# Kernel tuning notes

Hardware: AMD Instinct MI355X
Metric: run time of the kernel (lower is better)

The kernel has to match this reference:

```python
import jax, jax.numpy as jnp
import numpy as np

B, S, E, H = 4, 2048, 1024, 16
D = E // H  # head dim = 64


def setup_inputs() -> dict:
    key = jax.random.key(0)
    ks = jax.random.split(key, 8)
    scale = 0.02
    return {
        "query": jax.random.normal(ks[0], (B, S, E), jnp.float32),
        "keys": jax.random.normal(ks[1], (B, S, E), jnp.float32),
        "values": jax.random.normal(ks[2], (B, S, E), jnp.float32),
        "mask": jnp.ones((B, 1, 1, S), jnp.int32),
        "Wq": jax.random.normal(ks[3], (D, D), jnp.float32) * scale,
        "Wk": jax.random.normal(ks[4], (D, D), jnp.float32) * scale,
        "Wv": jax.random.normal(ks[5], (D, D), jnp.float32) * scale,
        "Wf": jax.random.normal(ks[6], (E, E), jnp.float32) * scale,
        "bf": jax.random.normal(ks[7], (E,), jnp.float32) * scale,
    }


def reference(query, keys, values, mask, Wq, Wk, Wv, Wf, bf):
    b, sq, _ = query.shape
    sk = keys.shape[1]
    # reshape to heads: [b, s, H, D]
    q = query.reshape(b, sq, H, D)
    k = keys.reshape(b, sk, H, D)
    v = values.reshape(b, sk, H, D)
    # per-head linear projections (torch Linear: x @ W.T, no bias)
    q = jnp.einsum('bshd,ed->bshe', q, Wq)
    k = jnp.einsum('bshd,ed->bshe', k, Wk)
    v = jnp.einsum('bshd,ed->bshe', v, Wv)
    # scores [b, h, q, k]
    scores = jnp.einsum('bqhd,bkhd->bhqk', q, k)
    scores = jnp.where(mask == 0, -jnp.inf, scores)
    attn = jax.nn.softmax(scores / jnp.sqrt(jnp.float32(D)), axis=3)
    # context [b, q, h, d] -> [b, q, E]
    ctx = jnp.einsum('bhqk,bkhd->bqhd', attn, v).reshape(b, sq, E)
    return ctx @ Wf.T + bf
```

## Files before the change

kernel.cpp:

```cpp
#include <hip/hip_runtime.h>

#define B_ 4
#define S_ 2048
#define E_ 1024
#define H_ 16
#define D_ 64

typedef unsigned short u16;
typedef unsigned int u32;
typedef __bf16 bf16x8 __attribute__((ext_vector_type(8)));
typedef __bf16 bf16x4 __attribute__((ext_vector_type(4)));
typedef float f32x4 __attribute__((ext_vector_type(4)));
typedef u16 u16x8 __attribute__((ext_vector_type(8)));
typedef u16 u16x4 __attribute__((ext_vector_type(4)));

#if defined(__has_builtin)
#if __has_builtin(__builtin_amdgcn_exp2f)
#define EXP2F(x) __builtin_amdgcn_exp2f(x)
#else
#define EXP2F(x) exp2f(x)
#endif
#else
#define EXP2F(x) exp2f(x)
#endif

__device__ __forceinline__ u16 bfbits(float f) {
  __bf16 h = (__bf16)f;
  return __builtin_bit_cast(u16, h);
}
__device__ __forceinline__ f32x4 mfma16(bf16x8 a, bf16x8 b, f32x4 c) {
  return __builtin_amdgcn_mfma_f32_16x16x32_bf16(a, b, c, 0, 0, 0);
}
__device__ __forceinline__ bf16x8 lds_ld8(const u16* base, int off) {
  return *reinterpret_cast<const bf16x8*>(reinterpret_cast<const char*>(base) + off);
}
__device__ __forceinline__ bf16x4 lds_ld4(const u16* base, int off) {
  return *reinterpret_cast<const bf16x4*>(reinterpret_cast<const char*>(base) + off);
}
__device__ __forceinline__ void gload_lds16(const u16* g, u16* l) {
  __builtin_amdgcn_global_load_lds((const __attribute__((address_space(1))) void*)g,
                                   (__attribute__((address_space(3))) void*)l, 16, 0, 0);
}

__global__ __launch_bounds__(256) void proj_kernel(
    const float* __restrict__ qin, const float* __restrict__ kin, const float* __restrict__ vin,
    const float* __restrict__ Wq, const float* __restrict__ Wk, const float* __restrict__ Wv,
    u16* __restrict__ qo, u16* __restrict__ ko, u16* __restrict__ vo)
{
  __shared__ __align__(16) u16 Al[128 * 64];
  __shared__ __align__(16) u16 Wl[64 * 64];
  const int t = threadIdx.x, w = t >> 6, l = t & 63, lg = l >> 4, ln = l & 15;
  const int tensor = blockIdx.z >> 2, b = blockIdx.z & 3;
  const int h = blockIdx.y, s0 = blockIdx.x * 128;

  const float* x; const float* W; float scale;
  if (tensor == 0)      { x = qin; W = Wq; scale = 0.125f * 1.44269504f; }
  else if (tensor == 1) { x = kin; W = Wk; scale = 1.0f; }
  else                  { x = vin; W = Wv; scale = 1.0f; }

  {
    const int e = t >> 2, d0 = (t & 3) * 16;
    const float4* wr = reinterpret_cast<const float4*>(W + e * 64 + d0);
    float4 f0 = wr[0], f1 = wr[1], f2 = wr[2], f3 = wr[3];
    u16x8 p0, p1;
    p0[0]=bfbits(f0.x*scale); p0[1]=bfbits(f0.y*scale); p0[2]=bfbits(f0.z*scale); p0[3]=bfbits(f0.w*scale);
    p0[4]=bfbits(f1.x*scale); p0[5]=bfbits(f1.y*scale); p0[6]=bfbits(f1.z*scale); p0[7]=bfbits(f1.w*scale);
    p1[0]=bfbits(f2.x*scale); p1[1]=bfbits(f2.y*scale); p1[2]=bfbits(f2.z*scale); p1[3]=bfbits(f2.w*scale);
    p1[4]=bfbits(f3.x*scale); p1[5]=bfbits(f3.y*scale); p1[6]=bfbits(f3.z*scale); p1[7]=bfbits(f3.w*scale);
    *reinterpret_cast<u16x8*>(reinterpret_cast<char*>(Wl) + ((e*128 + d0*2     ) ^ ((e & 7) << 4))) = p0;
    *reinterpret_cast<u16x8*>(reinterpret_cast<char*>(Wl) + ((e*128 + d0*2 + 16) ^ ((e & 7) << 4))) = p1;
  }
  {
    const int row = t >> 1, d0 = (t & 1) * 32;
    const float4* xr = reinterpret_cast<const float4*>(x + ((size_t)(b * S_ + s0 + row)) * E_ + h * D_ + d0);
    #pragma unroll
    for (int c = 0; c < 4; ++c) {
      float4 f0 = xr[2 * c], f1 = xr[2 * c + 1];
      u16x8 pk;
      pk[0]=bfbits(f0.x); pk[1]=bfbits(f0.y); pk[2]=bfbits(f0.z); pk[3]=bfbits(f0.w);
      pk[4]=bfbits(f1.x); pk[5]=bfbits(f1.y); pk[6]=bfbits(f1.z); pk[7]=bfbits(f1.w);
      *reinterpret_cast<u16x8*>(reinterpret_cast<char*>(Al) +
          ((row * 128 + (d0 + 8 * c) * 2) ^ ((row & 7) << 4))) = pk;
    }
  }
  __syncthreads();

  bf16x8 wb[4][2];
  #pragma unroll
  for (int nn = 0; nn < 4; ++nn) {
    int brow = nn * 16 + ln;
    int bo = (brow * 128 + lg * 16) ^ ((ln & 7) << 4);
    wb[nn][0] = lds_ld8(Wl, bo);
    wb[nn][1] = lds_ld8(Wl, bo ^ 64);
  }
  f32x4 acc[2][4] = {};
  #pragma unroll
  for (int sub = 0; sub < 2; ++sub) {
    int arow = 32 * w + 16 * sub + ln;
    int ao = (arow * 128 + lg * 16) ^ ((ln & 7) << 4);
    bf16x8 a0 = lds_ld8(Al, ao), a1 = lds_ld8(Al, ao ^ 64);
    #pragma unroll
    for (int nn = 0; nn < 4; ++nn) {
      acc[sub][nn] = mfma16(a0, wb[nn][0], acc[sub][nn]);
      acc[sub][nn] = mfma16(a1, wb[nn][1], acc[sub][nn]);
    }
  }

  if (tensor < 2) {
    u16* o = (tensor == 0) ? qo : ko;
    const size_t hb = ((size_t)(b * H_ + h)) * (S_ * D_);
    #pragma unroll
    for (int sub = 0; sub < 2; ++sub)
      #pragma unroll
      for (int nn = 0; nn < 4; ++nn)
        #pragma unroll
        for (int r = 0; r < 4; ++r)
          o[hb + (size_t)(s0 + 32*w + 16*sub + 4*lg + r) * D_ + nn*16 + ln] = bfbits(acc[sub][nn][r]);
  } else {
    const size_t hb = ((size_t)(b * H_ + h)) * (D_ * S_);
    #pragma unroll
    for (int sub = 0; sub < 2; ++sub)
      #pragma unroll
      for (int nn = 0; nn < 4; ++nn)
        #pragma unroll
        for (int r = 0; r < 4; ++r)
          vo[hb + (size_t)(nn*16 + ln) * S_ + s0 + 32*w + 16*sub + 4*lg + r] = bfbits(acc[sub][nn][r]);
  }
}

__global__ __launch_bounds__(256) void cvt_kernel(const float* __restrict__ in, u16* __restrict__ o)
{
  int i = blockIdx.x * 256 + threadIdx.x;
  float4 f = reinterpret_cast<const float4*>(in)[i];
  u16x4 h4;
  h4[0] = bfbits(f.x); h4[1] = bfbits(f.y); h4[2] = bfbits(f.z); h4[3] = bfbits(f.w);
  reinterpret_cast<u16x4*>(o)[i] = h4;
}

__global__ __launch_bounds__(512, 4) void attn_kernel(
    const u16* __restrict__ qw,
    const u16* __restrict__ kw,
    const u16* __restrict__ vtw,
    const int* __restrict__ mask,
    u16* __restrict__ ctx)
{
  __shared__ __align__(16) u16 Kl[2][64 * 64];
  __shared__ __align__(16) u16 Vl[2][64 * 64];
  __shared__ int s_allone;

  const int t = threadIdx.x, w = t >> 6, l = t & 63, lg = l >> 4, ln = l & 15;
  const int hb = blockIdx.x;
  const int b = hb >> 4;
  const int q0 = blockIdx.y * 256;
  const size_t koff = (size_t)hb * (S_ * D_);
  const size_t voff = (size_t)hb * (D_ * S_);

  if (t == 0) s_allone = 1;
  __syncthreads();

  const int srow = t >> 3, scol = (t & 7) ^ ((t >> 3) & 7);
  const u16* kg = kw + koff + srow * D_ + scol * 8;
  const u16* vg = vtw + voff + (size_t)srow * S_ + scol * 8;
  u16* kd = &Kl[0][0] + t * 8;
  u16* vd = &Vl[0][0] + t * 8;

  gload_lds16(kg, kd);
  gload_lds16(vg, vd);

  {
    const int4 m4 = *reinterpret_cast<const int4*>(mask + b * S_ + t * 4);
    if (!(m4.x && m4.y && m4.z && m4.w)) s_allone = 0;
  }

  bf16x8 qb[2][2];
  #pragma unroll
  for (int sub = 0; sub < 2; ++sub) {
    const u16* qp = qw + koff + (size_t)(q0 + 32*w + 16*sub + ln) * D_ + 8*lg;
    qb[sub][0] = *reinterpret_cast<const bf16x8*>(qp);
    qb[sub][1] = *reinterpret_cast<const bf16x8*>(qp + 32);
  }

  f32x4 oacc[2][4] = {};
  float l_s[2] = {0.f, 0.f};

  asm volatile("s_waitcnt vmcnt(0)" ::: "memory");
  __syncthreads();
  const int allone = s_allone;

  int cur = 0;
  for (int kt = 0; kt < S_ / 64; ++kt) {
    if (kt + 1 < S_ / 64) {
      const int nk = (kt + 1) * 64;
      gload_lds16(kg + nk * D_, kd + (cur ^ 1) * 4096);
      gload_lds16(vg + nk,      vd + (cur ^ 1) * 4096);
    }
    const u16* Kc = &Kl[cur][0];
    const u16* Vc = &Vl[cur][0];

    f32x4 sc[2][4];
    __builtin_amdgcn_s_setprio(1);
    #pragma unroll
    for (int kn = 0; kn < 4; ++kn) {
      int o0 = (ln * 128 + lg * 16) ^ ((ln & 7) << 4);
      o0 += kn * 2048;
      bf16x8 ka0 = lds_ld8(Kc, o0), ka1 = lds_ld8(Kc, o0 ^ 64);
      #pragma unroll
      for (int sub = 0; sub < 2; ++sub) {
        f32x4 z = {0.f, 0.f, 0.f, 0.f};
        z = mfma16(ka0, qb[sub][0], z);
        z = mfma16(ka1, qb[sub][1], z);
        sc[sub][kn] = z;
      }
    }
    __builtin_amdgcn_s_setprio(0);

    if (!allone) {
      const int kv0 = kt * 64;
      #pragma unroll
      for (int kn = 0; kn < 4; ++kn) {
        const int4 m4 = *reinterpret_cast<const int4*>(mask + b * S_ + kv0 + kn * 16 + lg * 4);
        const int* mp = reinterpret_cast<const int*>(&m4);
        #pragma unroll
        for (int r = 0; r < 4; ++r)
          if (mp[r] == 0) { sc[0][kn][r] = -1e30f; sc[1][kn][r] = -1e30f; }
      }
    }

    bf16x8 pa[2][2];
    #pragma unroll
    for (int sub = 0; sub < 2; ++sub) {
      float ps = 0.f;
      #pragma unroll
      for (int kn = 0; kn < 4; ++kn)
        #pragma unroll
        for (int r = 0; r < 4; ++r) {
          float p = EXP2F(sc[sub][kn][r]);
          ps += p;
          pa[sub][kn >> 1][(kn & 1) * 4 + r] = (__bf16)p;
        }
      l_s[sub] += ps;
    }

    __builtin_amdgcn_s_setprio(1);
    #pragma unroll
    for (int kh = 0; kh < 2; ++kh) {
      bf16x8 vb[4];
      #pragma unroll
      for (int dn = 0; dn < 4; ++dn) {
        int vo0 = ((ln * 128 + 8 * lg + 64 * kh) ^ ((ln & 7) << 4)) + dn * 2048;
        bf16x4 v0 = lds_ld4(Vc, vo0);
        bf16x4 v1 = lds_ld4(Vc, vo0 ^ 32);
        vb[dn] = __builtin_shufflevector(v0, v1, 0, 1, 2, 3, 4, 5, 6, 7);
      }
      #pragma unroll
      for (int sub = 0; sub < 2; ++sub)
        #pragma unroll
        for (int dn = 0; dn < 4; ++dn)
          oacc[sub][dn] = mfma16(pa[sub][kh], vb[dn], oacc[sub][dn]);
    }
    __builtin_amdgcn_s_setprio(0);

    if (kt + 1 < S_ / 64) {
      asm volatile("s_waitcnt vmcnt(0)" ::: "memory");
      __syncthreads();
      cur ^= 1;
    }
  }

  #pragma unroll
  for (int sub = 0; sub < 2; ++sub) {
    l_s[sub] += __shfl_xor(l_s[sub], 16, 64);
    l_s[sub] += __shfl_xor(l_s[sub], 32, 64);
    float linv = 1.f / l_s[sub];
    #pragma unroll
    for (int r = 0; r < 4; ++r) {
      float lr = __shfl(linv, 4 * lg + r, 64);
      int qrow = q0 + 32 * w + 16 * sub + 4 * lg + r;
      size_t base = ((size_t)b * S_ + qrow) * E_ + (hb & 15) * D_;
      #pragma unroll
      for (int dn = 0; dn < 4; ++dn)
        ctx[base + dn * 16 + ln] = bfbits(oacc[sub][dn][r] * lr);
    }
  }
}

__global__ __launch_bounds__(256, 2) void outproj_kernel(
    const u16* __restrict__ ctx, const u16* __restrict__ wf,
    const float* __restrict__ bias, float* __restrict__ out)
{
  __shared__ __align__(16) u16 Al[2][128 * 64];
  __shared__ __align__(16) u16 Bl[2][128 * 64];
  const int t = threadIdx.x, w = t >> 6, l = t & 63, lg = l >> 4, ln = l & 15;
  const int wm = w >> 1, wn = w & 1;
  const int m0 = blockIdx.x * 128, n0 = blockIdx.y * 128;
  f32x4 acc[4][4] = {};

  const u16* ag[4]; const u16* bg[4]; int ldo[4];
  #pragma unroll
  for (int it = 0; it < 4; ++it) {
    int j = it * 256 + t, row = j >> 3, c = (j & 7) ^ (row & 7);
    ag[it] = ctx + (size_t)(m0 + row) * E_ + c * 8;
    bg[it] = wf  + (size_t)(n0 + row) * E_ + c * 8;
    ldo[it] = j * 8;
  }
  #pragma unroll
  for (int it = 0; it < 4; ++it) {
    gload_lds16(ag[it], &Al[0][0] + ldo[it]);
    gload_lds16(bg[it], &Bl[0][0] + ldo[it]);
  }
  asm volatile("s_waitcnt vmcnt(0)" ::: "memory");
  __syncthreads();

  int cur = 0;
  for (int kt = 0; kt < E_ / 64; ++kt) {
    if (kt + 1 < E_ / 64) {
      const int k0 = (kt + 1) * 64;
      #pragma unroll
      for (int it = 0; it < 4; ++it) {
        gload_lds16(ag[it] + k0, &Al[cur ^ 1][0] + ldo[it]);
        gload_lds16(bg[it] + k0, &Bl[cur ^ 1][0] + ldo[it]);
      }
    }
    const u16* Ac = &Al[cur][0]; const u16* Bc = &Bl[cur][0];

    bf16x8 af[4][2], bff[4][2];
    #pragma unroll
    for (int ms = 0; ms < 4; ++ms) {
      int ar = 64 * wm + 16 * ms + ln;
      int ao = (ar * 128 + lg * 16) ^ ((ln & 7) << 4);
      af[ms][0] = lds_ld8(Ac, ao); af[ms][1] = lds_ld8(Ac, ao ^ 64);
    }
    #pragma unroll
    for (int ns = 0; ns < 4; ++ns) {
      int br = 64 * wn + 16 * ns + ln;
      int bo = (br * 128 + lg * 16) ^ ((ln & 7) << 4);
      bff[ns][0] = lds_ld8(Bc, bo); bff[ns][1] = lds_ld8(Bc, bo ^ 64);
    }
    __builtin_amdgcn_s_setprio(1);
    #pragma unroll
    for (int ms = 0; ms < 4; ++ms)
      #pragma unroll
      for (int ns = 0; ns < 4; ++ns) {
        acc[ms][ns] = mfma16(af[ms][0], bff[ns][0], acc[ms][ns]);
        acc[ms][ns] = mfma16(af[ms][1], bff[ns][1], acc[ms][ns]);
      }
    __builtin_amdgcn_s_setprio(0);

    if (kt + 1 < E_ / 64) {
      asm volatile("s_waitcnt vmcnt(0)" ::: "memory");
      __syncthreads();
      cur ^= 1;
    }
  }

  #pragma unroll
  for (int ns = 0; ns < 4; ++ns) {
    float bv = bias[n0 + 64 * wn + 16 * ns + ln];
    #pragma unroll
    for (int ms = 0; ms < 4; ++ms)
      #pragma unroll
      for (int r = 0; r < 4; ++r)
        out[(size_t)(m0 + 64*wm + 16*ms + 4*lg + r) * E_ + n0 + 64*wn + 16*ns + ln] =
            acc[ms][ns][r] + bv;
  }
}

extern "C" void kernel_launch(void* const* d_in, const int* in_sizes, int n_in,
                              void* d_out, int out_size, void* d_ws, size_t ws_size,
                              hipStream_t stream)
{
  const float* q   = (const float*)d_in[0];
  const float* k   = (const float*)d_in[1];
  const float* v   = (const float*)d_in[2];
  const int*  mask = (const int*) d_in[3];
  const float* Wq  = (const float*)d_in[4];
  const float* Wk  = (const float*)d_in[5];
  const float* Wv  = (const float*)d_in[6];
  const float* Wf  = (const float*)d_in[7];
  const float* bfv = (const float*)d_in[8];
  float* out = (float*)d_out;

  const size_t NQKV = (size_t)B_ * H_ * S_ * D_;
  const size_t NCTX = (size_t)B_ * S_ * E_;
  u16* q_ws   = (u16*)d_ws;
  u16* k_ws   = q_ws + NQKV;
  u16* v_ws   = k_ws + NQKV;
  u16* ctx_ws = v_ws + NQKV;
  u16* wf_ws  = ctx_ws + NCTX;

  proj_kernel<<<dim3(S_ / 128, H_, B_ * 3), dim3(256), 0, stream>>>(
      q, k, v, Wq, Wk, Wv, q_ws, k_ws, v_ws);
  cvt_kernel<<<dim3((E_ * E_) / 1024), dim3(256), 0, stream>>>(Wf, wf_ws);
  attn_kernel<<<dim3(B_ * H_, S_ / 256), dim3(512), 0, stream>>>(
      q_ws, k_ws, v_ws, mask, ctx_ws);
  outproj_kernel<<<dim3((B_ * S_) / 128, E_ / 128), dim3(256), 0, stream>>>(
      ctx_ws, wf_ws, bfv, out);
}
```

Before: 130.6 us.

## Halve attention query tile per block and compute row sums via MFMA

Each wave now handles 16 query rows instead of 32, the grid doubles along the query axis, and launch bounds ask for 8 blocks per CU for higher occupancy. The softmax denominator is accumulated with an MFMA against a ones vector in bf16 instead of scalar adds plus cross-lane shuffles. The cost is that each K/V tile loaded into LDS is reused by half as many query rows, which doubles K/V global traffic. Summing bf16-rounded probabilities also changes numerics slightly.

```diff
diff --git a/kernel.cpp b/kernel.cpp
--- a/kernel.cpp
+++ b/kernel.cpp
@@ -137,7 +137,7 @@
   reinterpret_cast<u16x4*>(o)[i] = h4;
 }
 
-__global__ __launch_bounds__(512, 4) void attn_kernel(
+__global__ __launch_bounds__(512, 8) void attn_kernel(
     const u16* __restrict__ qw,
     const u16* __restrict__ kw,
     const u16* __restrict__ vtw,
@@ -151,7 +151,7 @@
   const int t = threadIdx.x, w = t >> 6, l = t & 63, lg = l >> 4, ln = l & 15;
   const int hb = blockIdx.x;
   const int b = hb >> 4;
-  const int q0 = blockIdx.y * 256;
+  const int q0 = blockIdx.y * 128;
   const size_t koff = (size_t)hb * (S_ * D_);
   const size_t voff = (size_t)hb * (D_ * S_);
 
@@ -172,16 +172,20 @@
     if (!(m4.x && m4.y && m4.z && m4.w)) s_allone = 0;
   }
 
-  bf16x8 qb[2][2];
-  #pragma unroll
-  for (int sub = 0; sub < 2; ++sub) {
-    const u16* qp = qw + koff + (size_t)(q0 + 32*w + 16*sub + ln) * D_ + 8*lg;
-    qb[sub][0] = *reinterpret_cast<const bf16x8*>(qp);
-    qb[sub][1] = *reinterpret_cast<const bf16x8*>(qp + 32);
-  }
-
-  f32x4 oacc[2][4] = {};
-  float l_s[2] = {0.f, 0.f};
+  bf16x8 qb0, qb1;
+  {
+    const u16* qp = qw + koff + (size_t)(q0 + 16 * w + ln) * D_ + 8 * lg;
+    qb0 = *reinterpret_cast<const bf16x8*>(qp);
+    qb1 = *reinterpret_cast<const bf16x8*>(qp + 32);
+  }
+
+  u16x8 ob; 
+  #pragma unroll
+  for (int i = 0; i < 8; ++i) ob[i] = 0x3F80;
+  const bf16x8 ones = __builtin_bit_cast(bf16x8, ob);
+
+  f32x4 oacc[4] = {};
+  f32x4 lacc = {};
 
   asm volatile("s_waitcnt vmcnt(0)" ::: "memory");
   __syncthreads();
@@ -197,20 +201,16 @@
     const u16* Kc = &Kl[cur][0];
     const u16* Vc = &Vl[cur][0];
 
-    f32x4 sc[2][4];
+    f32x4 sc[4];
     __builtin_amdgcn_s_setprio(1);
     #pragma unroll
     for (int kn = 0; kn < 4; ++kn) {
-      int o0 = (ln * 128 + lg * 16) ^ ((ln & 7) << 4);
-      o0 += kn * 2048;
+      int o0 = ((ln * 128 + lg * 16) ^ ((ln & 7) << 4)) + kn * 2048;
       bf16x8 ka0 = lds_ld8(Kc, o0), ka1 = lds_ld8(Kc, o0 ^ 64);
-      #pragma unroll
-      for (int sub = 0; sub < 2; ++sub) {
-        f32x4 z = {0.f, 0.f, 0.f, 0.f};
-        z = mfma16(ka0, qb[sub][0], z);
-        z = mfma16(ka1, qb[sub][1], z);
-        sc[sub][kn] = z;
-      }
+      f32x4 z = {0.f, 0.f, 0.f, 0.f};
+      z = mfma16(ka0, qb0, z);
+      z = mfma16(ka1, qb1, z);
+      sc[kn] = z;
     }
     __builtin_amdgcn_s_setprio(0);
 
@@ -222,41 +222,30 @@
         const int* mp = reinterpret_cast<const int*>(&m4);
         #pragma unroll
         for (int r = 0; r < 4; ++r)
-          if (mp[r] == 0) { sc[0][kn][r] = -1e30f; sc[1][kn][r] = -1e30f; }
+          if (mp[r] == 0) sc[kn][r] = -1e30f;
       }
     }
 
-    bf16x8 pa[2][2];
-    #pragma unroll
-    for (int sub = 0; sub < 2; ++sub) {
-      float ps = 0.f;
-      #pragma unroll
-      for (int kn = 0; kn < 4; ++kn)
-        #pragma unroll
-        for (int r = 0; r < 4; ++r) {
-          float p = EXP2F(sc[sub][kn][r]);
-          ps += p;
-          pa[sub][kn >> 1][(kn & 1) * 4 + r] = (__bf16)p;
-        }
-      l_s[sub] += ps;
-    }
+    bf16x8 pa[2];
+    #pragma unroll
+    for (int kn = 0; kn < 4; ++kn)
+      #pragma unroll
+      for (int r = 0; r < 4; ++r)
+        pa[kn >> 1][(kn & 1) * 4 + r] = (__bf16)EXP2F(sc[kn][r]);
 
     __builtin_amdgcn_s_setprio(1);
+    lacc = mfma16(pa[0], ones, lacc);
+    lacc = mfma16(pa[1], ones, lacc);
     #pragma unroll
     for (int kh = 0; kh < 2; ++kh) {
-      bf16x8 vb[4];
       #pragma unroll
       for (int dn = 0; dn < 4; ++dn) {
         int vo0 = ((ln * 128 + 8 * lg + 64 * kh) ^ ((ln & 7) << 4)) + dn * 2048;
         bf16x4 v0 = lds_ld4(Vc, vo0);
         bf16x4 v1 = lds_ld4(Vc, vo0 ^ 32);
-        vb[dn] = __builtin_shufflevector(v0, v1, 0, 1, 2, 3, 4, 5, 6, 7);
+        bf16x8 vb = __builtin_shufflevector(v0, v1, 0, 1, 2, 3, 4, 5, 6, 7);
+        oacc[dn] = mfma16(pa[kh], vb, oacc[dn]);
       }
-      #pragma unroll
-      for (int sub = 0; sub < 2; ++sub)
-        #pragma unroll
-        for (int dn = 0; dn < 4; ++dn)
-          oacc[sub][dn] = mfma16(pa[sub][kh], vb[dn], oacc[sub][dn]);
     }
     __builtin_amdgcn_s_setprio(0);
 
@@ -268,19 +257,13 @@
   }
 
   #pragma unroll
-  for (int sub = 0; sub < 2; ++sub) {
-    l_s[sub] += __shfl_xor(l_s[sub], 16, 64);
-    l_s[sub] += __shfl_xor(l_s[sub], 32, 64);
-    float linv = 1.f / l_s[sub];
-    #pragma unroll
-    for (int r = 0; r < 4; ++r) {
-      float lr = __shfl(linv, 4 * lg + r, 64);
-      int qrow = q0 + 32 * w + 16 * sub + 4 * lg + r;
-      size_t base = ((size_t)b * S_ + qrow) * E_ + (hb & 15) * D_;
-      #pragma unroll
-      for (int dn = 0; dn < 4; ++dn)
-        ctx[base + dn * 16 + ln] = bfbits(oacc[sub][dn][r] * lr);
-    }
+  for (int r = 0; r < 4; ++r) {
+    float linv = 1.f / lacc[r];
+    int qrow = q0 + 16 * w + 4 * lg + r;
+    size_t base = ((size_t)b * S_ + qrow) * E_ + (hb & 15) * D_;
+    #pragma unroll
+    for (int dn = 0; dn < 4; ++dn)
+      ctx[base + dn * 16 + ln] = bfbits(oacc[dn][r] * linv);
   }
 }
 
@@ -391,7 +374,7 @@
   proj_kernel<<<dim3(S_ / 128, H_, B_ * 3), dim3(256), 0, stream>>>(
       q, k, v, Wq, Wk, Wv, q_ws, k_ws, v_ws);
   cvt_kernel<<<dim3((E_ * E_) / 1024), dim3(256), 0, stream>>>(Wf, wf_ws);
-  attn_kernel<<<dim3(B_ * H_, S_ / 256), dim3(512), 0, stream>>>(
+  attn_kernel<<<dim3(B_ * H_, S_ / 128), dim3(512), 0, stream>>>(
       q_ws, k_ws, v_ws, mask, ctx_ws);
   outproj_kernel<<<dim3((B_ * S_) / 128, E_ / 128), dim3(256), 0, stream>>>(
       ctx_ws, wf_ws, bfv, out);
```

Measured after the change: 149.1 us. 14.2% more time.

## Restructure attention to 4 warps with 64 rows each and MFMA row sums

Applied to the files above, without the earlier changes.

The attention kernel now uses 256 threads per block, with each warp owning 64 query rows instead of 32. This doubles reuse of each K/V LDS fragment across MFMAs, and each thread issues two async loads per tile. The softmax denominator is now computed with MFMA against a ones vector instead of scalar adds and cross-lane shuffles. V is written in a permuted column order so that one 16-byte LDS read replaces two 8-byte reads. The Wf bf16 conversion is folded into the projection launch as extra blocks, removing a separate kernel launch. In exchange, register pressure rises (larger accumulators) and occupancy per block changes.

```diff
diff --git a/kernel.cpp b/kernel.cpp
--- a/kernel.cpp
+++ b/kernel.cpp
@@ -9,7 +9,6 @@
 typedef unsigned short u16;
 typedef unsigned int u32;
 typedef __bf16 bf16x8 __attribute__((ext_vector_type(8)));
-typedef __bf16 bf16x4 __attribute__((ext_vector_type(4)));
 typedef float f32x4 __attribute__((ext_vector_type(4)));
 typedef u16 u16x8 __attribute__((ext_vector_type(8)));
 typedef u16 u16x4 __attribute__((ext_vector_type(4)));
@@ -34,9 +33,6 @@
 __device__ __forceinline__ bf16x8 lds_ld8(const u16* base, int off) {
   return *reinterpret_cast<const bf16x8*>(reinterpret_cast<const char*>(base) + off);
 }
-__device__ __forceinline__ bf16x4 lds_ld4(const u16* base, int off) {
-  return *reinterpret_cast<const bf16x4*>(reinterpret_cast<const char*>(base) + off);
-}
 __device__ __forceinline__ void gload_lds16(const u16* g, u16* l) {
   __builtin_amdgcn_global_load_lds((const __attribute__((address_space(1))) void*)g,
                                    (__attribute__((address_space(3))) void*)l, 16, 0, 0);
@@ -45,12 +41,25 @@
 __global__ __launch_bounds__(256) void proj_kernel(
     const float* __restrict__ qin, const float* __restrict__ kin, const float* __restrict__ vin,
     const float* __restrict__ Wq, const float* __restrict__ Wk, const float* __restrict__ Wv,
-    u16* __restrict__ qo, u16* __restrict__ ko, u16* __restrict__ vo)
+    const float* __restrict__ Wf,
+    u16* __restrict__ qo, u16* __restrict__ ko, u16* __restrict__ vo, u16* __restrict__ wfo)
 {
+  const int t = threadIdx.x;
+  const int tensor = blockIdx.z >> 2, b = blockIdx.z & 3;
+
+  if (tensor == 3) {
+    int chunk = ((blockIdx.z & 3) * 16 + blockIdx.y) * 16 + blockIdx.x;
+    int i = chunk * 256 + t;
+    float4 f = reinterpret_cast<const float4*>(Wf)[i];
+    u16x4 h4;
+    h4[0] = bfbits(f.x); h4[1] = bfbits(f.y); h4[2] = bfbits(f.z); h4[3] = bfbits(f.w);
+    reinterpret_cast<u16x4*>(wfo)[i] = h4;
+    return;
+  }
+
   __shared__ __align__(16) u16 Al[128 * 64];
   __shared__ __align__(16) u16 Wl[64 * 64];
-  const int t = threadIdx.x, w = t >> 6, l = t & 63, lg = l >> 4, ln = l & 15;
-  const int tensor = blockIdx.z >> 2, b = blockIdx.z & 3;
+  const int w = t >> 6, l = t & 63, lg = l >> 4, ln = l & 15;
   const int h = blockIdx.y, s0 = blockIdx.x * 128;
 
   const float* x; const float* W; float scale;
@@ -123,21 +132,16 @@
       #pragma unroll
       for (int nn = 0; nn < 4; ++nn)
         #pragma unroll
-        for (int r = 0; r < 4; ++r)
-          vo[hb + (size_t)(nn*16 + ln) * S_ + s0 + 32*w + 16*sub + 4*lg + r] = bfbits(acc[sub][nn][r]);
-  }
-}
-
-__global__ __launch_bounds__(256) void cvt_kernel(const float* __restrict__ in, u16* __restrict__ o)
-{
-  int i = blockIdx.x * 256 + threadIdx.x;
-  float4 f = reinterpret_cast<const float4*>(in)[i];
-  u16x4 h4;
-  h4[0] = bfbits(f.x); h4[1] = bfbits(f.y); h4[2] = bfbits(f.z); h4[3] = bfbits(f.w);
-  reinterpret_cast<u16x4*>(o)[i] = h4;
-}
-
-__global__ __launch_bounds__(512, 4) void attn_kernel(
+        for (int r = 0; r < 4; ++r) {
+          int scol = s0 + 32*w + 16*sub + 4*lg + r;
+          int sl = scol & 63;
+          int c = (sl & 3) | (((sl >> 4) & 1) << 2) | (((sl >> 2) & 3) << 3) | ((sl >> 5) << 5);
+          vo[hb + (size_t)(nn*16 + ln) * S_ + (scol & ~63) + c] = bfbits(acc[sub][nn][r]);
+        }
+  }
+}
+
+__global__ __launch_bounds__(256, 2) void attn_kernel(
     const u16* __restrict__ qw,
     const u16* __restrict__ kw,
     const u16* __restrict__ vtw,
@@ -165,23 +169,31 @@
   u16* vd = &Vl[0][0] + t * 8;
 
   gload_lds16(kg, kd);
+  gload_lds16(kg + 32 * D_, kd + 2048);
   gload_lds16(vg, vd);
+  gload_lds16(vg + (size_t)32 * S_, vd + 2048);
 
   {
-    const int4 m4 = *reinterpret_cast<const int4*>(mask + b * S_ + t * 4);
-    if (!(m4.x && m4.y && m4.z && m4.w)) s_allone = 0;
-  }
-
-  bf16x8 qb[2][2];
-  #pragma unroll
-  for (int sub = 0; sub < 2; ++sub) {
-    const u16* qp = qw + koff + (size_t)(q0 + 32*w + 16*sub + ln) * D_ + 8*lg;
+    const int4 m0 = *reinterpret_cast<const int4*>(mask + b * S_ + t * 8);
+    const int4 m1 = *reinterpret_cast<const int4*>(mask + b * S_ + t * 8 + 4);
+    if (!(m0.x && m0.y && m0.z && m0.w && m1.x && m1.y && m1.z && m1.w)) s_allone = 0;
+  }
+
+  bf16x8 qb[4][2];
+  #pragma unroll
+  for (int sub = 0; sub < 4; ++sub) {
+    const u16* qp = qw + koff + (size_t)(q0 + 64*w + 16*sub + ln) * D_ + 8*lg;
     qb[sub][0] = *reinterpret_cast<const bf16x8*>(qp);
     qb[sub][1] = *reinterpret_cast<const bf16x8*>(qp + 32);
   }
 
-  f32x4 oacc[2][4] = {};
-  float l_s[2] = {0.f, 0.f};
+  u16x8 ob;
+  #pragma unroll
+  for (int i = 0; i < 8; ++i) ob[i] = 0x3F80;
+  const bf16x8 ones = __builtin_bit_cast(bf16x8, ob);
+
+  f32x4 oacc[4][4] = {};
+  f32x4 lacc[4] = {};
 
   asm volatile("s_waitcnt vmcnt(0)" ::: "memory");
   __syncthreads();
@@ -191,72 +203,72 @@
   for (int kt = 0; kt < S_ / 64; ++kt) {
     if (kt + 1 < S_ / 64) {
       const int nk = (kt + 1) * 64;
-      gload_lds16(kg + nk * D_, kd + (cur ^ 1) * 4096);
-      gload_lds16(vg + nk,      vd + (cur ^ 1) * 4096);
+      u16* kdn = kd + (cur ^ 1) * 4096;
+      u16* vdn = vd + (cur ^ 1) * 4096;
+      gload_lds16(kg + nk * D_, kdn);
+      gload_lds16(kg + (nk + 32) * D_, kdn + 2048);
+      gload_lds16(vg + nk, vdn);
+      gload_lds16(vg + (size_t)32 * S_ + nk, vdn + 2048);
     }
     const u16* Kc = &Kl[cur][0];
     const u16* Vc = &Vl[cur][0];
 
-    f32x4 sc[2][4];
+    bf16x8 pa[4][2];
+    #pragma unroll
+    for (int sp = 0; sp < 2; ++sp) {
+      f32x4 sc[2][4];
+      __builtin_amdgcn_s_setprio(1);
+      #pragma unroll
+      for (int kn = 0; kn < 4; ++kn) {
+        int o0 = ((ln * 128 + lg * 16) ^ ((ln & 7) << 4)) + kn * 2048;
+        bf16x8 ka0 = lds_ld8(Kc, o0), ka1 = lds_ld8(Kc, o0 ^ 64);
+        #pragma unroll
+        for (int s2 = 0; s2 < 2; ++s2) {
+          f32x4 z = {0.f, 0.f, 0.f, 0.f};
+          z = mfma16(ka0, qb[sp * 2 + s2][0], z);
+          z = mfma16(ka1, qb[sp * 2 + s2][1], z);
+          sc[s2][kn] = z;
+        }
+      }
+      __builtin_amdgcn_s_setprio(0);
+
+      if (!allone) {
+        const int kv0 = kt * 64;
+        #pragma unroll
+        for (int kn = 0; kn < 4; ++kn) {
+          const int4 m4 = *reinterpret_cast<const int4*>(mask + b * S_ + kv0 + kn * 16 + lg * 4);
+          const int* mp = reinterpret_cast<const int*>(&m4);
+          #pragma unroll
+          for (int r = 0; r < 4; ++r)
+            if (mp[r] == 0) { sc[0][kn][r] = -1e30f; sc[1][kn][r] = -1e30f; }
+        }
+      }
+
+      #pragma unroll
+      for (int s2 = 0; s2 < 2; ++s2)
+        #pragma unroll
+        for (int kn = 0; kn < 4; ++kn)
+          #pragma unroll
+          for (int r = 0; r < 4; ++r)
+            pa[sp * 2 + s2][kn >> 1][(kn & 1) * 4 + r] = (__bf16)EXP2F(sc[s2][kn][r]);
+    }
+
     __builtin_amdgcn_s_setprio(1);
     #pragma unroll
-    for (int kn = 0; kn < 4; ++kn) {
-      int o0 = (ln * 128 + lg * 16) ^ ((ln & 7) << 4);
-      o0 += kn * 2048;
-      bf16x8 ka0 = lds_ld8(Kc, o0), ka1 = lds_ld8(Kc, o0 ^ 64);
-      #pragma unroll
-      for (int sub = 0; sub < 2; ++sub) {
-        f32x4 z = {0.f, 0.f, 0.f, 0.f};
-        z = mfma16(ka0, qb[sub][0], z);
-        z = mfma16(ka1, qb[sub][1], z);
-        sc[sub][kn] = z;
+    for (int sub = 0; sub < 4; ++sub) {
+      lacc[sub] = mfma16(pa[sub][0], ones, lacc[sub]);
+      lacc[sub] = mfma16(pa[sub][1], ones, lacc[sub]);
+    }
+    #pragma unroll
+    for (int kh = 0; kh < 2; ++kh) {
+      #pragma unroll
+      for (int dn = 0; dn < 4; ++dn) {
+        int vo0 = ((ln * 128 + 16 * lg + 64 * kh) ^ ((ln & 7) << 4)) + dn * 2048;
+        bf16x8 vb = lds_ld8(Vc, vo0);
+        #pragma unroll
+        for (int sub = 0; sub < 4; ++sub)
+          oacc[sub][dn] = mfma16(pa[sub][kh], vb, oacc[sub][dn]);
       }
-    }
-    __builtin_amdgcn_s_setprio(0);
-
-    if (!allone) {
-      const int kv0 = kt * 64;
-      #pragma unroll
-      for (int kn = 0; kn < 4; ++kn) {
-        const int4 m4 = *reinterpret_cast<const int4*>(mask + b * S_ + kv0 + kn * 16 + lg * 4);
-        const int* mp = reinterpret_cast<const int*>(&m4);
-        #pragma unroll
-        for (int r = 0; r < 4; ++r)
-          if (mp[r] == 0) { sc[0][kn][r] = -1e30f; sc[1][kn][r] = -1e30f; }
-      }
-    }
-
-    bf16x8 pa[2][2];
-    #pragma unroll
-    for (int sub = 0; sub < 2; ++sub) {
-      float ps = 0.f;
-      #pragma unroll
-      for (int kn = 0; kn < 4; ++kn)
-        #pragma unroll
-        for (int r = 0; r < 4; ++r) {
-          float p = EXP2F(sc[sub][kn][r]);
-          ps += p;
-          pa[sub][kn >> 1][(kn & 1) * 4 + r] = (__bf16)p;
-        }
-      l_s[sub] += ps;
-    }
-
-    __builtin_amdgcn_s_setprio(1);
-    #pragma unroll
-    for (int kh = 0; kh < 2; ++kh) {
-      bf16x8 vb[4];
-      #pragma unroll
-      for (int dn = 0; dn < 4; ++dn) {
-        int vo0 = ((ln * 128 + 8 * lg + 64 * kh) ^ ((ln & 7) << 4)) + dn * 2048;
-        bf16x4 v0 = lds_ld4(Vc, vo0);
-        bf16x4 v1 = lds_ld4(Vc, vo0 ^ 32);
-        vb[dn] = __builtin_shufflevector(v0, v1, 0, 1, 2, 3, 4, 5, 6, 7);
-      }
-      #pragma unroll
-      for (int sub = 0; sub < 2; ++sub)
-        #pragma unroll
-        for (int dn = 0; dn < 4; ++dn)
-          oacc[sub][dn] = mfma16(pa[sub][kh], vb[dn], oacc[sub][dn]);
     }
     __builtin_amdgcn_s_setprio(0);
 
@@ -268,18 +280,15 @@
   }
 
   #pragma unroll
-  for (int sub = 0; sub < 2; ++sub) {
-    l_s[sub] += __shfl_xor(l_s[sub], 16, 64);
-    l_s[sub] += __shfl_xor(l_s[sub], 32, 64);
-    float linv = 1.f / l_s[sub];
+  for (int sub = 0; sub < 4; ++sub) {
     #pragma unroll
     for (int r = 0; r < 4; ++r) {
-      float lr = __shfl(linv, 4 * lg + r, 64);
-      int qrow = q0 + 32 * w + 16 * sub + 4 * lg + r;
+      float linv = 1.f / lacc[sub][r];
+      int qrow = q0 + 64 * w + 16 * sub + 4 * lg + r;
       size_t base = ((size_t)b * S_ + qrow) * E_ + (hb & 15) * D_;
       #pragma unroll
       for (int dn = 0; dn < 4; ++dn)
-        ctx[base + dn * 16 + ln] = bfbits(oacc[sub][dn][r] * lr);
+        ctx[base + dn * 16 + ln] = bfbits(oacc[sub][dn][r] * linv);
     }
   }
 }
@@ -388,10 +397,9 @@
   u16* ctx_ws = v_ws + NQKV;
   u16* wf_ws  = ctx_ws + NCTX;
 
-  proj_kernel<<<dim3(S_ / 128, H_, B_ * 3), dim3(256), 0, stream>>>(
-      q, k, v, Wq, Wk, Wv, q_ws, k_ws, v_ws);
-  cvt_kernel<<<dim3((E_ * E_) / 1024), dim3(256), 0, stream>>>(Wf, wf_ws);
-  attn_kernel<<<dim3(B_ * H_, S_ / 256), dim3(512), 0, stream>>>(
+  proj_kernel<<<dim3(S_ / 128, H_, 16), dim3(256), 0, stream>>>(
+      q, k, v, Wq, Wk, Wv, Wf, q_ws, k_ws, v_ws, wf_ws);
+  attn_kernel<<<dim3(B_ * H_, S_ / 256), dim3(256), 0, stream>>>(
       q_ws, k_ws, v_ws, mask, ctx_ws);
   outproj_kernel<<<dim3((B_ * S_) / 128, E_ / 128), dim3(256), 0, stream>>>(
       ctx_ws, wf_ws, bfv, out);
```

Result: faster. 118.8 us (-9.0%).
